# Performance work log

Hardware: AMD Instinct MI355X
Metric: run time of the kernel (lower is better)

Reference implementation:

```python
import jax, jax.numpy as jnp
import numpy as np

EPS = 1e-6
BANDWIDTH = 10


def _norm_last(x):
    return x / jnp.sum(x, axis=-1, keepdims=True)


def _causal_linear_branch(Q, K, V, eps):
    # Q,K: [N,L,H,E] feature-mapped; V: [N,L,H,D]
    Q = _norm_last(Q)
    K = _norm_last(K)
    Kcum = jnp.cumsum(K, axis=1)                                   # [N,L,H,E]
    Z = 1.0 / (jnp.einsum('nlhe,nlhe->nlh', Q, Kcum) + eps)        # [N,L,H]
    # causal_dot_product: running sum of outer products K_s V_s^T
    S = jnp.cumsum(K[..., :, None] * V[..., None, :], axis=1)       # [N,L,H,E,D]
    Vn = jnp.einsum('nlhe,nlhed->nlhd', Q, S)                       # [N,L,H,D]
    return Vn * Z[..., None]


def setup_inputs() -> dict:
    key = jax.random.key(0)
    k1, k2, k3, k4 = jax.random.split(key, 4)
    N, L, H, E = 2, 2048, 8, 32
    return {
        'queries': jax.random.normal(k1, (N, L, H, E), dtype=jnp.float32),
        'keys': jax.random.normal(k2, (N, L, H, E), dtype=jnp.float32),
        'values': jax.random.normal(k3, (N, L, H, E), dtype=jnp.float32),
        'key_lengths': jnp.ones((N, L), dtype=jnp.float32),
        'W1': 0.02 * jax.random.normal(k4, (1, 1, H, E), dtype=jnp.float32),
        'W2': jnp.ones((1, 1, H, E), dtype=jnp.float32) * 0.5,
        'W3': jnp.ones((1, 1, H, E), dtype=jnp.float32) * 0.5,
    }


def reference(queries, keys, values, key_lengths, W1, W2, W3):
    klen = key_lengths[:, :, None, None]
    # kernel 1: elu feature map phi(x) = elu(x) + 1
    Q1 = jax.nn.elu(queries) + 1.0
    K1 = (jax.nn.elu(keys) + 1.0) * klen
    LV = W2 * _causal_linear_branch(Q1, K1, values, EPS)
    # kernel 2: squared elu feature map phi(x) = (elu(x) + 1)^2
    Q2 = (jax.nn.elu(queries) + 1.0) ** 2
    K2 = ((jax.nn.elu(keys) + 1.0) ** 2) * klen
    LV = LV + W3 * _causal_linear_branch(Q2, K2, values, EPS)
    # sparse near-field: banded causal softmax attention
    N, L, H, E = queries.shape
    temp = 1.0 / np.sqrt(E).astype(np.float32)
    QK = jnp.einsum('nlhe,nshe->nhls', queries * temp, keys)       # [N,H,L,S]
    li = jnp.arange(L)[:, None]
    si = jnp.arange(L)[None, :]
    band = (si <= li) & (si > li - BANDWIDTH)                      # keep band of width `bandwidth`
    QK = jnp.where(band[None, None], QK, -jnp.inf)
    A = jax.nn.softmax(QK, axis=-1)                                # dropout is identity (p=0 / eval)
    SV = jnp.einsum('nhls,nshd->nlhd', A, values)
    return W1 * SV + LV
```

## Files before the change

kernel.cpp:

```cpp
#include <hip/hip_runtime.h>
#include <cmath>

constexpr int NN = 2;
constexpr int LL = 2048;
constexpr int HH = 8;
constexpr int EE = 32;
constexpr int CC = 32;
constexpr int NCH = LL / CC;
constexpr int NB  = NN * HH * NCH;
constexpr int BWD = 10;
constexpr float EPSF = 1e-6f;
constexpr int REC  = 2 * (EE * EE + EE);
constexpr int REC4 = REC / 4;
constexpr int OFF_S1 = 0, OFF_K1 = 1024, OFF_S2 = 1056, OFF_K2 = 2080;
constexpr int SK = EE + 4;


__device__ __forceinline__ float elu1(float x) {
    return x > 0.f ? x + 1.f : __expf(x);
}

__global__ __launch_bounds__(256) void chunksum_kernel(
    const float* __restrict__ Kin, const float* __restrict__ Vin,
    float* __restrict__ ws)
{
    __shared__ float K1n[CC][SK];
    __shared__ float K2n[CC][SK];
    __shared__ float Vs [CC][SK];

    const int b  = blockIdx.x;
    const int c  = b & (NCH - 1);
    const int nh = b >> 6;
    const int t  = threadIdx.x;
    const int lane = t & 31;
    const int grp  = t >> 5;

    for (int r = grp; r < CC; r += 8) {
        const int l = c * CC + r;
        const int base = ((nh >> 3) * LL + l) * HH * EE + (nh & 7) * EE + lane;
        const float k = Kin[base];
        const float v = Vin[base];
        const float f1 = elu1(k);
        const float f2 = f1 * f1;
        float s1 = f1, s2 = f2;
        #pragma unroll
        for (int m = 1; m < 32; m <<= 1) {
            s1 += __shfl_xor(s1, m, 32);
            s2 += __shfl_xor(s2, m, 32);
        }
        K1n[r][lane] = f1 / s1;
        K2n[r][lane] = f2 / s2;
        Vs [r][lane] = v;
    }
    __syncthreads();

    const int e  = t >> 3;
    const int d0 = (t & 7) * 4;
    float4 a1 = {0.f, 0.f, 0.f, 0.f};
    float4 a2 = {0.f, 0.f, 0.f, 0.f};
    float ks1 = 0.f, ks2 = 0.f;
    for (int j = 0; j < CC; ++j) {
        const float k1 = K1n[j][e];
        const float k2 = K2n[j][e];
        const float4 v = *(const float4*)&Vs[j][d0];
        ks1 += k1; ks2 += k2;
        a1.x += k1 * v.x; a1.y += k1 * v.y; a1.z += k1 * v.z; a1.w += k1 * v.w;
        a2.x += k2 * v.x; a2.y += k2 * v.y; a2.z += k2 * v.z; a2.w += k2 * v.w;
    }
    float* wb = ws + (size_t)b * REC;
    *(float4*)&wb[OFF_S1 + e * EE + d0] = a1;
    *(float4*)&wb[OFF_S2 + e * EE + d0] = a2;
    if ((t & 7) == 0) {
        wb[OFF_K1 + e] = ks1;
        wb[OFF_K2 + e] = ks2;
    }
}

__global__ __launch_bounds__(192) void prefix_kernel(float* __restrict__ ws)
{
    const int g = blockIdx.x / 11;
    const int e = (blockIdx.x % 11) * 192 + threadIdx.x;
    float* base = ws + (size_t)g * NCH * REC + e;
    float run = 0.f;
    {
        float v[32];
        #pragma unroll
        for (int c = 0; c < 32; ++c) v[c] = base[(size_t)c * REC];
        #pragma unroll
        for (int c = 0; c < 32; ++c) {
            const float x = v[c];
            base[(size_t)c * REC] = run;
            run += x;
        }
    }
    {
        float v[32];
        #pragma unroll
        for (int c = 0; c < 32; ++c) v[c] = base[(size_t)(32 + c) * REC];
        #pragma unroll
        for (int c = 0; c < 32; ++c) {
            const float x = v[c];
            base[(size_t)(32 + c) * REC] = run;
            run += x;
        }
    }
}

__global__ __launch_bounds__(256) void fused_kernel(
    const float* __restrict__ Qin, const float* __restrict__ Kin,
    const float* __restrict__ Vin,
    const float* __restrict__ W1, const float* __restrict__ W2,
    const float* __restrict__ W3, const float* __restrict__ ws,
    float* __restrict__ out)
{
    __shared__ float Kf [CC][SK];
    __shared__ float Vs [CC + 9][SK];
    __shared__ float Qf [CC][SK];
    __shared__ float ki1[CC], ki2[CC], qi1[CC], qi2[CC];
    __shared__ __align__(16) union {
        float kr[(CC + 9) * SK];
        float sp[REC];
    } U;

    const int b  = blockIdx.x;
    const int c  = b & (NCH - 1);
    const int nh = b >> 6;
    const int h  = nh & 7;
    const int n  = nh >> 3;
    const int l0 = c * CC;
    const int t  = threadIdx.x;
    const int lane = t & 31;
    const int grp  = t >> 5;

    const float4* wbv = (const float4*)(ws + (size_t)b * REC);
    const float4 s0 = wbv[t];
    const float4 s1 = wbv[256 + t];
    float4 s2 = {0.f, 0.f, 0.f, 0.f};
    if (t < REC4 - 512) s2 = wbv[512 + t];

    for (int r = grp; r < CC; r += 8) {
        const int l = l0 + r;
        const int base = ((n * LL + l) * HH + h) * EE + lane;
        const float k = Kin[base];
        const float v = Vin[base];
        const float q = Qin[base];
        const float fk = elu1(k), fk2 = fk * fk;
        const float fq = elu1(q), fq2 = fq * fq;
        float sk1 = fk, sk2 = fk2, sq1 = fq, sq2 = fq2;
        #pragma unroll
        for (int m = 1; m < 32; m <<= 1) {
            sk1 += __shfl_xor(sk1, m, 32);
            sk2 += __shfl_xor(sk2, m, 32);
            sq1 += __shfl_xor(sq1, m, 32);
            sq2 += __shfl_xor(sq2, m, 32);
        }
        Kf[r][lane] = fk;
        Qf[r][lane] = fq;
        Vs[9 + r][lane] = v;
        U.kr[(9 + r) * SK + lane] = k;
        if (lane == 0) {
            ki1[r] = 1.f / sk1; ki2[r] = 1.f / sk2;
            qi1[r] = 1.f / sq1; qi2[r] = 1.f / sq2;
        }
    }
    for (int idx = t; idx < 9 * 32; idx += 256) {
        const int rr = idx >> 5, ln = idx & 31;
        const int l = l0 - 9 + rr;
        float kv = 0.f, vv = 0.f;
        if (l >= 0) {
            const int base = ((n * LL + l) * HH + h) * EE + ln;
            kv = Kin[base];
            vv = Vin[base];
        }
        U.kr[rr * SK + ln] = kv;
        Vs[rr][ln] = vv;
    }

    const int r   = t >> 3;
    const int sub = t & 7;
    const int d0  = sub * 4;
    const int l   = l0 + r;

    const float4 q4 = *(const float4*)&Qin[((n * LL + l) * HH + h) * EE + d0];
    __syncthreads();

    float bnd[4];
    {
        const float temp = 0.17677669529663687f;
        float mx = -INFINITY, den = 0.f;
        float sv0 = 0.f, sv1 = 0.f, sv2 = 0.f, sv3 = 0.f;
        #pragma unroll
        for (int jj = 0; jj < BWD; ++jj) {
            const int j = l - (BWD - 1) + jj;
            if (j >= 0) {
                const float4 k4 = *(const float4*)&U.kr[(r + jj) * SK + d0];
                float p = q4.x*k4.x + q4.y*k4.y + q4.z*k4.z + q4.w*k4.w;
                p += __shfl_xor(p, 1, 8); p += __shfl_xor(p, 2, 8); p += __shfl_xor(p, 4, 8);
                const float s  = p * temp;
                const float mn = fmaxf(mx, s);
                const float c1 = __expf(mx - mn);
                const float c2 = __expf(s - mn);
                const float4 v4 = *(const float4*)&Vs[r + jj][d0];
                den = den * c1 + c2;
                sv0 = sv0 * c1 + c2 * v4.x;
                sv1 = sv1 * c1 + c2 * v4.y;
                sv2 = sv2 * c1 + c2 * v4.z;
                sv3 = sv3 * c1 + c2 * v4.w;
                mx = mn;
            }
        }
        const float inv = 1.f / den;
        const float4 w1 = *(const float4*)&W1[h * EE + d0];
        bnd[0] = w1.x * sv0 * inv; bnd[1] = w1.y * sv1 * inv;
        bnd[2] = w1.z * sv2 * inv; bnd[3] = w1.w * sv3 * inv;
    }
    __syncthreads();

    ((float4*)U.sp)[t]       = s0;
    ((float4*)U.sp)[256 + t] = s1;
    if (t < REC4 - 512) ((float4*)U.sp)[512 + t] = s2;
    __syncthreads();

    const float* S1p = U.sp + OFF_S1;
    const float* S2p = U.sp + OFF_S2;
    const float* k1p = U.sp + OFF_K1;
    const float* k2p = U.sp + OFF_K2;

    const float qi1v = qi1[r];
    const float qi2v = qi2[r];
    float4 qf4;
    qf4.x = elu1(q4.x); qf4.y = elu1(q4.y);
    qf4.z = elu1(q4.z); qf4.w = elu1(q4.w);

    float a1[4] = {0.f, 0.f, 0.f, 0.f};
    float a2[4] = {0.f, 0.f, 0.f, 0.f};
    float dp1 = 0.f, dp2 = 0.f;

    #pragma unroll 4
    for (int e = 0; e < EE; ++e) {
        const float tq  = Qf[r][e];
        const float tq2 = tq * tq;
        dp1 += tq  * k1p[e];
        dp2 += tq2 * k2p[e];
        const float4 sa = *(const float4*)&S1p[e * EE + d0];
        const float4 ta = *(const float4*)&S2p[e * EE + d0];
        a1[0] += tq  * sa.x; a1[1] += tq  * sa.y; a1[2] += tq  * sa.z; a1[3] += tq  * sa.w;
        a2[0] += tq2 * ta.x; a2[1] += tq2 * ta.y; a2[2] += tq2 * ta.z; a2[3] += tq2 * ta.w;
    }

    for (int j = 0; j <= r; ++j) {
        const float4 kf = *(const float4*)&Kf[j][d0];
        const float t0 = qf4.x * kf.x, t1 = qf4.y * kf.y;
        const float t2 = qf4.z * kf.z, t3 = qf4.w * kf.w;
        float u1 = (t0 + t1) + (t2 + t3);
        float u2 = ((t0 * t0 + t1 * t1) + (t2 * t2 + t3 * t3));
        u1 += __shfl_xor(u1, 1, 8); u1 += __shfl_xor(u1, 2, 8); u1 += __shfl_xor(u1, 4, 8);
        u2 += __shfl_xor(u2, 1, 8); u2 += __shfl_xor(u2, 2, 8); u2 += __shfl_xor(u2, 4, 8);
        const float p1 = u1 * ki1[j];
        const float p2 = u2 * ki2[j];
        dp1 += p1;
        dp2 += p2;
        const float4 va = *(const float4*)&Vs[9 + j][d0];
        a1[0] += p1 * va.x; a1[1] += p1 * va.y; a1[2] += p1 * va.z; a1[3] += p1 * va.w;
        a2[0] += p2 * va.x; a2[1] += p2 * va.y; a2[2] += p2 * va.z; a2[3] += p2 * va.w;
    }

    const float z1 = qi1v / (qi1v * dp1 + EPSF);
    const float z2 = qi2v / (qi2v * dp2 + EPSF);
    const float4 w2 = *(const float4*)&W2[h * EE + d0];
    const float4 w3 = *(const float4*)&W3[h * EE + d0];
    float4 o;
    o.x = bnd[0] + w2.x * a1[0] * z1 + w3.x * a2[0] * z2;
    o.y = bnd[1] + w2.y * a1[1] * z1 + w3.y * a2[1] * z2;
    o.z = bnd[2] + w2.z * a1[2] * z1 + w3.z * a2[2] * z2;
    o.w = bnd[3] + w2.w * a1[3] * z1 + w3.w * a2[3] * z2;
    *(float4*)&out[((n * LL + l) * HH + h) * EE + d0] = o;
}

extern "C" void kernel_launch(void* const* d_in, const int* in_sizes, int n_in,
                              void* d_out, int out_size, void* d_ws, size_t ws_size,
                              hipStream_t stream)
{
    const float* Q  = (const float*)d_in[0];
    const float* K  = (const float*)d_in[1];
    const float* V  = (const float*)d_in[2];
    const float* W1 = (const float*)d_in[4];
    const float* W2 = (const float*)d_in[5];
    const float* W3 = (const float*)d_in[6];
    float* out = (float*)d_out;
    float* ws  = (float*)d_ws;

    chunksum_kernel<<<NB,           256, 0, stream>>>(K, V, ws);
    prefix_kernel  <<<NN * HH * 11, 192, 0, stream>>>(ws);
    fused_kernel   <<<NB,           256, 0, stream>>>(Q, K, V, W1, W2, W3, ws, out);
}
```

Measured before the change: 106.2 us.

## Merge three kernels into one persistent kernel with grid-wide atomic barriers

Replaces the chunk-sum, prefix-scan and fused output kernels with a single kernel that synchronises all blocks through atomic spin barriers in the workspace. Each block computes its chunk's K⊗V sums from the shared-memory tiles it already loaded, then the grid scans them in place, then each block finishes its outputs. Raw queries are cached in shared memory instead of being reloaded. This removes launch gaps and redundant K/V loads, but relies on all 1024 blocks being co-resident. It also relies on barrier-counter reset ordering being safe across repeated calls.

```diff
diff --git a/kernel.cpp b/kernel.cpp
--- a/kernel.cpp
+++ b/kernel.cpp
@@ -14,108 +14,40 @@
 constexpr int REC4 = REC / 4;
 constexpr int OFF_S1 = 0, OFF_K1 = 1024, OFF_S2 = 1056, OFF_K2 = 2080;
 constexpr int SK = EE + 4;
+constexpr int NSCAN = NN * HH * REC;
+constexpr unsigned MAGIC = 0x13579BDFu;
 
 
 __device__ __forceinline__ float elu1(float x) {
     return x > 0.f ? x + 1.f : __expf(x);
 }
 
-__global__ __launch_bounds__(256) void chunksum_kernel(
-    const float* __restrict__ Kin, const float* __restrict__ Vin,
-    float* __restrict__ ws)
-{
-    __shared__ float K1n[CC][SK];
-    __shared__ float K2n[CC][SK];
-    __shared__ float Vs [CC][SK];
-
-    const int b  = blockIdx.x;
-    const int c  = b & (NCH - 1);
-    const int nh = b >> 6;
-    const int t  = threadIdx.x;
-    const int lane = t & 31;
-    const int grp  = t >> 5;
-
-    for (int r = grp; r < CC; r += 8) {
-        const int l = c * CC + r;
-        const int base = ((nh >> 3) * LL + l) * HH * EE + (nh & 7) * EE + lane;
-        const float k = Kin[base];
-        const float v = Vin[base];
-        const float f1 = elu1(k);
-        const float f2 = f1 * f1;
-        float s1 = f1, s2 = f2;
-        #pragma unroll
-        for (int m = 1; m < 32; m <<= 1) {
-            s1 += __shfl_xor(s1, m, 32);
-            s2 += __shfl_xor(s2, m, 32);
-        }
-        K1n[r][lane] = f1 / s1;
-        K2n[r][lane] = f2 / s2;
-        Vs [r][lane] = v;
-    }
-    __syncthreads();
-
-    const int e  = t >> 3;
-    const int d0 = (t & 7) * 4;
-    float4 a1 = {0.f, 0.f, 0.f, 0.f};
-    float4 a2 = {0.f, 0.f, 0.f, 0.f};
-    float ks1 = 0.f, ks2 = 0.f;
-    for (int j = 0; j < CC; ++j) {
-        const float k1 = K1n[j][e];
-        const float k2 = K2n[j][e];
-        const float4 v = *(const float4*)&Vs[j][d0];
-        ks1 += k1; ks2 += k2;
-        a1.x += k1 * v.x; a1.y += k1 * v.y; a1.z += k1 * v.z; a1.w += k1 * v.w;
-        a2.x += k2 * v.x; a2.y += k2 * v.y; a2.z += k2 * v.z; a2.w += k2 * v.w;
-    }
-    float* wb = ws + (size_t)b * REC;
-    *(float4*)&wb[OFF_S1 + e * EE + d0] = a1;
-    *(float4*)&wb[OFF_S2 + e * EE + d0] = a2;
-    if ((t & 7) == 0) {
-        wb[OFF_K1 + e] = ks1;
-        wb[OFF_K2 + e] = ks2;
-    }
-}
-
-__global__ __launch_bounds__(192) void prefix_kernel(float* __restrict__ ws)
-{
-    const int g = blockIdx.x / 11;
-    const int e = (blockIdx.x % 11) * 192 + threadIdx.x;
-    float* base = ws + (size_t)g * NCH * REC + e;
-    float run = 0.f;
-    {
-        float v[32];
-        #pragma unroll
-        for (int c = 0; c < 32; ++c) v[c] = base[(size_t)c * REC];
-        #pragma unroll
-        for (int c = 0; c < 32; ++c) {
-            const float x = v[c];
-            base[(size_t)c * REC] = run;
-            run += x;
-        }
-    }
-    {
-        float v[32];
-        #pragma unroll
-        for (int c = 0; c < 32; ++c) v[c] = base[(size_t)(32 + c) * REC];
-        #pragma unroll
-        for (int c = 0; c < 32; ++c) {
-            const float x = v[c];
-            base[(size_t)(32 + c) * REC] = run;
-            run += x;
-        }
-    }
-}
-
-__global__ __launch_bounds__(256) void fused_kernel(
+__device__ __forceinline__ void spin_until_eq(unsigned* p, unsigned val) {
+    int spins = 0;
+    while (__hip_atomic_load(p, __ATOMIC_RELAXED, __HIP_MEMORY_SCOPE_AGENT) != val) {
+        __builtin_amdgcn_s_sleep(2);
+        if (++spins > 3000000) break;
+    }
+}
+__device__ __forceinline__ void spin_until_ge(unsigned* p, unsigned val) {
+    int spins = 0;
+    while (__hip_atomic_load(p, __ATOMIC_RELAXED, __HIP_MEMORY_SCOPE_AGENT) < val) {
+        __builtin_amdgcn_s_sleep(2);
+        if (++spins > 3000000) break;
+    }
+}
+
+__global__ __launch_bounds__(256, 4) void mono_kernel(
     const float* __restrict__ Qin, const float* __restrict__ Kin,
     const float* __restrict__ Vin,
     const float* __restrict__ W1, const float* __restrict__ W2,
-    const float* __restrict__ W3, const float* __restrict__ ws,
+    const float* __restrict__ W3, float* __restrict__ ws,
     float* __restrict__ out)
 {
     __shared__ float Kf [CC][SK];
+    __shared__ float Qf [CC][SK];
+    __shared__ float Qr [CC][SK];
     __shared__ float Vs [CC + 9][SK];
-    __shared__ float Qf [CC][SK];
     __shared__ float ki1[CC], ki2[CC], qi1[CC], qi2[CC];
     __shared__ __align__(16) union {
         float kr[(CC + 9) * SK];
@@ -132,11 +64,12 @@
     const int lane = t & 31;
     const int grp  = t >> 5;
 
-    const float4* wbv = (const float4*)(ws + (size_t)b * REC);
-    const float4 s0 = wbv[t];
-    const float4 s1 = wbv[256 + t];
-    float4 s2 = {0.f, 0.f, 0.f, 0.f};
-    if (t < REC4 - 512) s2 = wbv[512 + t];
+    unsigned* bar = (unsigned*)(ws + (size_t)NB * REC);
+    if (b == 0 && t == 0) {
+        __hip_atomic_store(&bar[0],  0u,    __ATOMIC_RELAXED, __HIP_MEMORY_SCOPE_AGENT);
+        __hip_atomic_store(&bar[16], 0u,    __ATOMIC_RELAXED, __HIP_MEMORY_SCOPE_AGENT);
+        __hip_atomic_store(&bar[32], MAGIC, __ATOMIC_RELEASE, __HIP_MEMORY_SCOPE_AGENT);
+    }
 
     for (int r = grp; r < CC; r += 8) {
         const int l = l0 + r;
@@ -156,6 +89,7 @@
         }
         Kf[r][lane] = fk;
         Qf[r][lane] = fq;
+        Qr[r][lane] = q;
         Vs[9 + r][lane] = v;
         U.kr[(9 + r) * SK + lane] = k;
         if (lane == 0) {
@@ -168,21 +102,101 @@
         const int l = l0 - 9 + rr;
         float kv = 0.f, vv = 0.f;
         if (l >= 0) {
-            const int base = ((n * LL + l) * HH + h) * EE + ln;
-            kv = Kin[base];
-            vv = Vin[base];
+            const int gbase = ((n * LL + l) * HH + h) * EE + ln;
+            kv = Kin[gbase];
+            vv = Vin[gbase];
         }
         U.kr[rr * SK + ln] = kv;
         Vs[rr][ln] = vv;
     }
+    __syncthreads();
+
+    {
+        const int e  = t >> 3;
+        const int d0 = (t & 7) * 4;
+        float4 a1 = {0.f, 0.f, 0.f, 0.f};
+        float4 a2 = {0.f, 0.f, 0.f, 0.f};
+        float ks1 = 0.f, ks2 = 0.f;
+        for (int j = 0; j < CC; ++j) {
+            const float kf = Kf[j][e];
+            const float p1 = kf * ki1[j];
+            const float p2 = kf * kf * ki2[j];
+            const float4 v = *(const float4*)&Vs[9 + j][d0];
+            ks1 += p1; ks2 += p2;
+            a1.x += p1 * v.x; a1.y += p1 * v.y; a1.z += p1 * v.z; a1.w += p1 * v.w;
+            a2.x += p2 * v.x; a2.y += p2 * v.y; a2.z += p2 * v.z; a2.w += p2 * v.w;
+        }
+        float* wb = ws + (size_t)b * REC;
+        *(float4*)&wb[OFF_S1 + e * EE + d0] = a1;
+        *(float4*)&wb[OFF_S2 + e * EE + d0] = a2;
+        if ((t & 7) == 0) {
+            wb[OFF_K1 + e] = ks1;
+            wb[OFF_K2 + e] = ks2;
+        }
+    }
+
+    __syncthreads();
+    if (t == 0) {
+        __threadfence();
+        spin_until_eq(&bar[32], MAGIC);
+        __hip_atomic_fetch_add(&bar[0], 1u, __ATOMIC_ACQ_REL, __HIP_MEMORY_SCOPE_AGENT);
+        spin_until_ge(&bar[0], (unsigned)NB);
+        __threadfence();
+    }
+    __syncthreads();
+
+    {
+        const int gt = b * 256 + t;
+        if (gt < NSCAN) {
+            const int g = gt / REC;
+            const int e = gt - g * REC;
+            float* basep = ws + (size_t)g * NCH * REC + e;
+            float run = 0.f;
+            {
+                float v[32];
+                #pragma unroll
+                for (int cc = 0; cc < 32; ++cc) v[cc] = basep[(size_t)cc * REC];
+                #pragma unroll
+                for (int cc = 0; cc < 32; ++cc) {
+                    const float x = v[cc];
+                    basep[(size_t)cc * REC] = run;
+                    run += x;
+                }
+            }
+            {
+                float v[32];
+                #pragma unroll
+                for (int cc = 0; cc < 32; ++cc) v[cc] = basep[(size_t)(32 + cc) * REC];
+                #pragma unroll
+                for (int cc = 0; cc < 32; ++cc) {
+                    const float x = v[cc];
+                    basep[(size_t)(32 + cc) * REC] = run;
+                    run += x;
+                }
+            }
+        }
+    }
+
+    __syncthreads();
+    if (t == 0) {
+        __threadfence();
+        __hip_atomic_fetch_add(&bar[16], 1u, __ATOMIC_ACQ_REL, __HIP_MEMORY_SCOPE_AGENT);
+        spin_until_ge(&bar[16], (unsigned)NB);
+        __threadfence();
+    }
+    __syncthreads();
+
+    const float4* wbv = (const float4*)(ws + (size_t)b * REC);
+    const float4 s0 = wbv[t];
+    const float4 s1 = wbv[256 + t];
+    float4 s2 = {0.f, 0.f, 0.f, 0.f};
+    if (t < REC4 - 512) s2 = wbv[512 + t];
 
     const int r   = t >> 3;
     const int sub = t & 7;
     const int d0  = sub * 4;
     const int l   = l0 + r;
-
-    const float4 q4 = *(const float4*)&Qin[((n * LL + l) * HH + h) * EE + d0];
-    __syncthreads();
+    const float4 q4 = *(const float4*)&Qr[r][d0];
 
     float bnd[4];
     {
@@ -281,6 +295,7 @@
                               void* d_out, int out_size, void* d_ws, size_t ws_size,
                               hipStream_t stream)
 {
+    (void)in_sizes; (void)n_in; (void)out_size; (void)ws_size;
     const float* Q  = (const float*)d_in[0];
     const float* K  = (const float*)d_in[1];
     const float* V  = (const float*)d_in[2];
@@ -290,7 +305,5 @@
     float* out = (float*)d_out;
     float* ws  = (float*)d_ws;
 
-    chunksum_kernel<<<NB,           256, 0, stream>>>(K, V, ws);
-    prefix_kernel  <<<NN * HH * 11, 192, 0, stream>>>(ws);
-    fused_kernel   <<<NB,           256, 0, stream>>>(Q, K, V, W1, W2, W3, ws, out);
-}
+    mono_kernel<<<NB, 256, 0, stream>>>(Q, K, V, W1, W2, W3, ws, out);
+}
```

New measurement: 316.3 us. +197.8%, slower.

## Compute intra-chunk linear attention and state contraction with bf16 MFMA

Applied to the files above, without the earlier changes.

Replaces the per-thread scalar loops for the intra-chunk causal QK^T·V product and the Q·S inter-chunk state contraction with bf16 32x32x16 MFMA instructions. Two wavefronts each handle one feature-map branch, and normalizer dot products are also computed via MFMA with a ones vector. Keys are pre-normalized and stored as bf16 in shared memory, and results are staged through shared buffers before the final combine. This trades fp32 precision for bf16 and leaves half the wavefronts idle during the MFMA phase, adding an extra barrier.

```diff
diff --git a/kernel.cpp b/kernel.cpp
--- a/kernel.cpp
+++ b/kernel.cpp
@@ -14,10 +14,21 @@
 constexpr int REC4 = REC / 4;
 constexpr int OFF_S1 = 0, OFF_K1 = 1024, OFF_S2 = 1056, OFF_K2 = 2080;
 constexpr int SK = EE + 4;
-
+constexpr int SB = 40;
+
+using f32x16 = __attribute__((ext_vector_type(16))) float;
+using s16x8  = __attribute__((ext_vector_type(8)))  short;
 
 __device__ __forceinline__ float elu1(float x) {
     return x > 0.f ? x + 1.f : __expf(x);
+}
+__device__ __forceinline__ unsigned short bfr(float x) {
+    union { float f; unsigned u; } v; v.f = x;
+    return (unsigned short)((v.u + 0x7FFFu + ((v.u >> 16) & 1u)) >> 16);
+}
+__device__ __forceinline__ float bf2f(unsigned short b) {
+    union { unsigned u; float f; } v; v.u = ((unsigned)b) << 16;
+    return v.f;
 }
 
 __global__ __launch_bounds__(256) void chunksum_kernel(
@@ -113,10 +124,15 @@
     const float* __restrict__ W3, const float* __restrict__ ws,
     float* __restrict__ out)
 {
-    __shared__ float Kf [CC][SK];
     __shared__ float Vs [CC + 9][SK];
-    __shared__ float Qf [CC][SK];
-    __shared__ float ki1[CC], ki2[CC], qi1[CC], qi2[CC];
+    __shared__ float qi1[CC], qi2[CC];
+    __shared__ __align__(16) unsigned short Qfb [CC][SB];
+    __shared__ __align__(16) unsigned short K1nb[CC][SB];
+    __shared__ __align__(16) unsigned short K2nb[CC][SB];
+    __shared__ __align__(16) unsigned short Pb1 [CC][SB];
+    __shared__ __align__(16) unsigned short Pb2 [CC][SB];
+    __shared__ float Ob1[CC][SK];
+    __shared__ float Ob2[CC][SK];
     __shared__ __align__(16) union {
         float kr[(CC + 9) * SK];
         float sp[REC];
@@ -154,12 +170,14 @@
             sq1 += __shfl_xor(sq1, m, 32);
             sq2 += __shfl_xor(sq2, m, 32);
         }
-        Kf[r][lane] = fk;
-        Qf[r][lane] = fq;
+        const float is1 = __builtin_amdgcn_rcpf(sk1);
+        const float is2 = __builtin_amdgcn_rcpf(sk2);
+        Qfb [r][lane] = bfr(fq);
+        K1nb[r][lane] = bfr(fk  * is1);
+        K2nb[r][lane] = bfr(fk2 * is2);
         Vs[9 + r][lane] = v;
         U.kr[(9 + r) * SK + lane] = k;
         if (lane == 0) {
-            ki1[r] = 1.f / sk1; ki2[r] = 1.f / sk2;
             qi1[r] = 1.f / sq1; qi2[r] = 1.f / sq2;
         }
     }
@@ -168,9 +186,9 @@
         const int l = l0 - 9 + rr;
         float kv = 0.f, vv = 0.f;
         if (l >= 0) {
-            const int base = ((n * LL + l) * HH + h) * EE + ln;
-            kv = Kin[base];
-            vv = Vin[base];
+            const int gbase = ((n * LL + l) * HH + h) * EE + ln;
+            kv = Kin[gbase];
+            vv = Vin[gbase];
         }
         U.kr[rr * SK + ln] = kv;
         Vs[rr][ln] = vv;
@@ -221,59 +239,99 @@
     if (t < REC4 - 512) ((float4*)U.sp)[512 + t] = s2;
     __syncthreads();
 
-    const float* S1p = U.sp + OFF_S1;
-    const float* S2p = U.sp + OFF_S2;
-    const float* k1p = U.sp + OFF_K1;
-    const float* k2p = U.sp + OFF_K2;
-
-    const float qi1v = qi1[r];
-    const float qi2v = qi2[r];
-    float4 qf4;
-    qf4.x = elu1(q4.x); qf4.y = elu1(q4.y);
-    qf4.z = elu1(q4.z); qf4.w = elu1(q4.w);
-
-    float a1[4] = {0.f, 0.f, 0.f, 0.f};
-    float a2[4] = {0.f, 0.f, 0.f, 0.f};
-    float dp1 = 0.f, dp2 = 0.f;
-
-    #pragma unroll 4
-    for (int e = 0; e < EE; ++e) {
-        const float tq  = Qf[r][e];
-        const float tq2 = tq * tq;
-        dp1 += tq  * k1p[e];
-        dp2 += tq2 * k2p[e];
-        const float4 sa = *(const float4*)&S1p[e * EE + d0];
-        const float4 ta = *(const float4*)&S2p[e * EE + d0];
-        a1[0] += tq  * sa.x; a1[1] += tq  * sa.y; a1[2] += tq  * sa.z; a1[3] += tq  * sa.w;
-        a2[0] += tq2 * ta.x; a2[1] += tq2 * ta.y; a2[2] += tq2 * ta.z; a2[3] += tq2 * ta.w;
-    }
-
-    for (int j = 0; j <= r; ++j) {
-        const float4 kf = *(const float4*)&Kf[j][d0];
-        const float t0 = qf4.x * kf.x, t1 = qf4.y * kf.y;
-        const float t2 = qf4.z * kf.z, t3 = qf4.w * kf.w;
-        float u1 = (t0 + t1) + (t2 + t3);
-        float u2 = ((t0 * t0 + t1 * t1) + (t2 * t2 + t3 * t3));
-        u1 += __shfl_xor(u1, 1, 8); u1 += __shfl_xor(u1, 2, 8); u1 += __shfl_xor(u1, 4, 8);
-        u2 += __shfl_xor(u2, 1, 8); u2 += __shfl_xor(u2, 2, 8); u2 += __shfl_xor(u2, 4, 8);
-        const float p1 = u1 * ki1[j];
-        const float p2 = u2 * ki2[j];
-        dp1 += p1;
-        dp2 += p2;
-        const float4 va = *(const float4*)&Vs[9 + j][d0];
-        a1[0] += p1 * va.x; a1[1] += p1 * va.y; a1[2] += p1 * va.z; a1[3] += p1 * va.w;
-        a2[0] += p2 * va.x; a2[1] += p2 * va.y; a2[2] += p2 * va.z; a2[3] += p2 * va.w;
-    }
-
-    const float z1 = qi1v / (qi1v * dp1 + EPSF);
-    const float z2 = qi2v / (qi2v * dp2 + EPSF);
-    const float4 w2 = *(const float4*)&W2[h * EE + d0];
-    const float4 w3 = *(const float4*)&W3[h * EE + d0];
+    const int wid = t >> 6;
+    const int l64 = t & 63;
+    const int l31 = l64 & 31;
+    const int hi5 = l64 >> 5;
+
+    if ((wid & 1) == 0) {
+        const bool b2 = (wid == 2);
+        const unsigned short* Kn = b2 ? &K2nb[0][0] : &K1nb[0][0];
+        const float* Sp  = U.sp + (b2 ? OFF_S2 : OFF_S1);
+        const float* kp  = U.sp + (b2 ? OFF_K2 : OFF_K1);
+        const float* qiv = b2 ? qi2 : qi1;
+        const float* Wv  = b2 ? W3  : W2;
+        unsigned short* Pb = b2 ? &Pb2[0][0] : &Pb1[0][0];
+        float* Ob = b2 ? &Ob2[0][0] : &Ob1[0][0];
+
+        s16x8 qa0 = *(const s16x8*)&Qfb[l31][8 * hi5];
+        s16x8 qa1 = *(const s16x8*)&Qfb[l31][16 + 8 * hi5];
+        if (b2) {
+            #pragma unroll
+            for (int i = 0; i < 8; ++i) {
+                const float f0 = bf2f((unsigned short)qa0[i]);
+                const float f1 = bf2f((unsigned short)qa1[i]);
+                qa0[i] = (short)bfr(f0 * f0);
+                qa1[i] = (short)bfr(f1 * f1);
+            }
+        }
+        const s16x8 kb0 = *(const s16x8*)&Kn[l31 * SB + 8 * hi5];
+        const s16x8 kb1 = *(const s16x8*)&Kn[l31 * SB + 16 + 8 * hi5];
+
+        f32x16 P = {};
+        P = __builtin_amdgcn_mfma_f32_32x32x16_bf16(qa0, kb0, P, 0, 0, 0);
+        P = __builtin_amdgcn_mfma_f32_32x32x16_bf16(qa1, kb1, P, 0, 0, 0);
+
+        #pragma unroll
+        for (int k = 0; k < 16; ++k) {
+            const int row = (k & 3) + 8 * (k >> 2) + 4 * hi5;
+            const float pv = (l31 <= row) ? P[k] : 0.f;
+            Pb[row * SB + l31] = bfr(pv);
+        }
+        const s16x8 pa0 = *(const s16x8*)&Pb[l31 * SB + 8 * hi5];
+        const s16x8 pa1 = *(const s16x8*)&Pb[l31 * SB + 16 + 8 * hi5];
+
+        s16x8 vb0, vb1;
+        #pragma unroll
+        for (int i = 0; i < 8; ++i) {
+            vb0[i] = (short)bfr(Vs[9 + 8 * hi5 + i][l31]);
+            vb1[i] = (short)bfr(Vs[9 + 16 + 8 * hi5 + i][l31]);
+        }
+        s16x8 sb0, sb1;
+        #pragma unroll
+        for (int i = 0; i < 8; ++i) {
+            sb0[i] = (short)bfr(Sp[(8 * hi5 + i) * EE + l31]);
+            sb1[i] = (short)bfr(Sp[(16 + 8 * hi5 + i) * EE + l31]);
+        }
+        f32x16 A = {};
+        A = __builtin_amdgcn_mfma_f32_32x32x16_bf16(pa0, vb0, A, 0, 0, 0);
+        A = __builtin_amdgcn_mfma_f32_32x32x16_bf16(pa1, vb1, A, 0, 0, 0);
+        A = __builtin_amdgcn_mfma_f32_32x32x16_bf16(qa0, sb0, A, 0, 0, 0);
+        A = __builtin_amdgcn_mfma_f32_32x32x16_bf16(qa1, sb1, A, 0, 0, 0);
+
+        s16x8 ones;
+        #pragma unroll
+        for (int i = 0; i < 8; ++i) ones[i] = (short)0x3F80;
+        s16x8 rb0, rb1;
+        #pragma unroll
+        for (int i = 0; i < 8; ++i) {
+            rb0[i] = (short)bfr(kp[8 * hi5 + i]);
+            rb1[i] = (short)bfr(kp[16 + 8 * hi5 + i]);
+        }
+        f32x16 Dp = {};
+        Dp = __builtin_amdgcn_mfma_f32_32x32x16_bf16(pa0, ones, Dp, 0, 0, 0);
+        Dp = __builtin_amdgcn_mfma_f32_32x32x16_bf16(pa1, ones, Dp, 0, 0, 0);
+        Dp = __builtin_amdgcn_mfma_f32_32x32x16_bf16(qa0, rb0, Dp, 0, 0, 0);
+        Dp = __builtin_amdgcn_mfma_f32_32x32x16_bf16(qa1, rb1, Dp, 0, 0, 0);
+
+        const float wv = Wv[h * EE + l31];
+        #pragma unroll
+        for (int k = 0; k < 16; ++k) {
+            const int row = (k & 3) + 8 * (k >> 2) + 4 * hi5;
+            const float qi = qiv[row];
+            const float z  = qi / (qi * Dp[k] + EPSF);
+            Ob[row * SK + l31] = wv * A[k] * z;
+        }
+    }
+    __syncthreads();
+
+    const float4 o1 = *(const float4*)&Ob1[r][d0];
+    const float4 o2 = *(const float4*)&Ob2[r][d0];
     float4 o;
-    o.x = bnd[0] + w2.x * a1[0] * z1 + w3.x * a2[0] * z2;
-    o.y = bnd[1] + w2.y * a1[1] * z1 + w3.y * a2[1] * z2;
-    o.z = bnd[2] + w2.z * a1[2] * z1 + w3.z * a2[2] * z2;
-    o.w = bnd[3] + w2.w * a1[3] * z1 + w3.w * a2[3] * z2;
+    o.x = bnd[0] + o1.x + o2.x;
+    o.y = bnd[1] + o1.y + o2.y;
+    o.z = bnd[2] + o1.z + o2.z;
+    o.w = bnd[3] + o1.w + o2.w;
     *(float4*)&out[((n * LL + l) * HH + h) * EE + d0] = o;
 }
 
@@ -281,6 +339,7 @@
                               void* d_out, int out_size, void* d_ws, size_t ws_size,
                               hipStream_t stream)
 {
+    (void)in_sizes; (void)n_in; (void)out_size; (void)ws_size;
     const float* Q  = (const float*)d_in[0];
     const float* K  = (const float*)d_in[1];
     const float* V  = (const float*)d_in[2];
```

Result: faster. 102.0 us (-4.0%).
